# Performance work log

Hardware: AMD Instinct MI355X
Metric: run time of the kernel (lower is better)

## Reference

```python
import jax, jax.numpy as jnp
import numpy as np

J = 24       # num_joints
DIM = 3      # point dim
CD = 128     # c_dim
BN = 4       # bottleneck_size
HPG = 32     # hidden per group (hidden_size=768 / 24)

def setup_inputs() -> dict:
    key = jax.random.key(0)
    ks = jax.random.split(key, 16)
    B, T = 4, 25000
    s = lambda k, shape, fan_in: jax.random.normal(k, shape, jnp.float32) * (1.0 / np.sqrt(fan_in))
    return {
        "p": jax.random.normal(ks[0], (B, J * DIM, T), jnp.float32),
        "z": jax.random.normal(ks[1], (B, 128), jnp.float32),
        "c": jax.random.normal(ks[2], (B, CD), jnp.float32),
        # grouped Conv1d weights stored as (J, out_per_group, in_per_group)
        "W_proj": s(ks[3], (J, BN, CD), CD),          "b_proj": jnp.zeros((J * BN,), jnp.float32),
        "W_p":   s(ks[4], (J, HPG, DIM + BN), DIM+BN), "b_p":   jnp.zeros((J * HPG,), jnp.float32),
        "W0":    s(ks[5], (J, HPG, HPG), HPG),         "b0":    jnp.zeros((J * HPG,), jnp.float32),
        "W1":    s(ks[6], (J, HPG, HPG), HPG),         "b1":    jnp.zeros((J * HPG,), jnp.float32),
        "W2":    s(ks[7], (J, HPG, HPG), HPG),         "b2":    jnp.zeros((J * HPG,), jnp.float32),
        "W_out": s(ks[8], (J, 1, HPG), HPG),           "b_out": jnp.zeros((J,), jnp.float32),
    }

def _gconv(x, W, b):
    # grouped 1x1 conv: x (B,J,Cin,T), W (J,Cout,Cin), b (J*Cout,) -> (B,J,Cout,T)
    y = jnp.einsum('bjit,joi->bjot', x, W)
    return y + b.reshape(1, J, -1, 1)

def reference(p, z, c, W_proj, b_proj, W_p, b_p, W0, b0, W1, b1, W2, b2, W_out, b_out):
    B, _, T = p.shape
    # p.view(B, J, -1, T) then keep last `dim` channels
    p_in = p.reshape(B, J, -1, T)[:, :, -DIM:, :]            # (B,J,3,T)
    # 2D c branch: repeat per joint, grouped proj, broadcast over T
    c_rep = jnp.broadcast_to(c[:, None, :], (B, J, CD))       # (B,J,128)
    c_proj = jnp.einsum('bjc,joc->bjo', c_rep, W_proj) + b_proj.reshape(1, J, BN)
    c_proj = jnp.broadcast_to(c_proj[:, :, :, None], (B, J, BN, T))
    x = jnp.concatenate([p_in, c_proj], axis=2)               # (B,J,3+4,T)
    net = jax.nn.relu(_gconv(x,   W_p, b_p))
    net = jax.nn.relu(_gconv(net, W0,  b0))
    net = jax.nn.relu(_gconv(net, W1,  b1))
    net = jax.nn.relu(_gconv(net, W2,  b2))
    out = _gconv(net, W_out, b_out)                           # (B,J,1,T)
    return out.reshape(B, J, T)                               # logits (B, num_joints, T)
```

## Files before the change

### kernel.cpp

```cpp
#include <hip/hip_runtime.h>
#include <hip/hip_bf16.h>

#define NJ 24
#define TLEN 25000
#define NB 4
#define CHUNKS 20
#define NWPB (CHUNKS*4)
#define NITERS ((TLEN+63)/64)

typedef short short8 __attribute__((ext_vector_type(8)));
typedef short s16x2 __attribute__((ext_vector_type(2)));
typedef float f32x16 __attribute__((ext_vector_type(16)));

union FragU { unsigned u[4]; short8 s; };

__device__ __forceinline__ unsigned pack2(float a, float b){
    unsigned ua = __float_as_uint(a) + 0x8000u;
    unsigned ub = __float_as_uint(b) + 0x8000u;
    return __builtin_amdgcn_perm(ub, ua, 0x07060302u);
}
__device__ __forceinline__ float bflo(unsigned u){
    union { unsigned v; float f; } t; t.v = u << 16; return t.f;
}

__device__ __forceinline__ unsigned pkrelu(unsigned x){
    union { unsigned u; s16x2 v; } a, r;
    a.u = x;
    s16x2 z; z[0] = 0; z[1] = 0;
    r.v = __builtin_elementwise_max(a.v, z);
    return r.u;
}

__device__ __forceinline__ f32x16 mfma(const FragU &a, const FragU &b, f32x16 c){
    return __builtin_amdgcn_mfma_f32_32x32x16_bf16(a.s, b.s, c, 0, 0, 0);
}

__device__ __forceinline__ FragU mk1(unsigned w){
    FragU f; f.u[0] = w; f.u[1] = 0; f.u[2] = 0; f.u[3] = 0; return f;
}

__device__ __forceinline__ void relu_pack(const f32x16 &acc, FragU &k0, FragU &k1){
    unsigned w[8];
    #pragma unroll
    for (int i = 0; i < 8; ++i) w[i] = pkrelu(pack2(acc[2*i], acc[2*i+1]));
    k0.u[0]=w[0]; k0.u[1]=w[1]; k0.u[2]=w[2]; k0.u[3]=w[3];
    k1.u[0]=w[4]; k1.u[1]=w[5]; k1.u[2]=w[6]; k1.u[3]=w[7];
}

__global__ __launch_bounds__(256, 2) void ptf_decoder_kernel(
    const float* __restrict__ p,    const float* __restrict__ c,
    const float* __restrict__ Wproj,const float* __restrict__ bproj,
    const float* __restrict__ Wp,   const float* __restrict__ bp,
    const float* __restrict__ W0,   const float* __restrict__ b0,
    const float* __restrict__ W1,   const float* __restrict__ b1,
    const float* __restrict__ W2,   const float* __restrict__ b2,
    const float* __restrict__ Wout, const float* __restrict__ bout,
    float* __restrict__ out)
{
    __shared__ __align__(16) float ldsW[3][32][36];
    __shared__ __align__(16) float ldsWp[32][8];
    __shared__ __align__(16) float ldsB[3][32];
    __shared__ __align__(16) float ldsWo[32];

    const int tid = threadIdx.x;
    const int bj  = blockIdx.x % (NB*NJ);
    const int sub = blockIdx.x / (NB*NJ);
    const int b   = bj / NJ;
    const int j   = bj % NJ;

    {
        const float* Wl[3] = {W0, W1, W2};
        #pragma unroll
        for (int L = 0; L < 3; ++L) {
            int row = tid >> 3, c4 = tid & 7;
            float4 v = *reinterpret_cast<const float4*>(Wl[L] + ((size_t)(j*32 + row))*32 + c4*4);
            *reinterpret_cast<float4*>(&ldsW[L][row][c4*4]) = v;
        }
        {
            int row = tid >> 3, i8 = tid & 7;
            ldsWp[row][i8] = (i8 < 7) ? Wp[((size_t)(j*32 + row))*7 + i8]
                                      : bp[j*32 + row];
        }
        if      (tid < 32)  ldsB[0][tid]      = b0[j*32 + tid];
        else if (tid < 64)  ldsB[1][tid-32]   = b1[j*32 + tid-32];
        else if (tid < 96)  ldsB[2][tid-64]   = b2[j*32 + tid-64];
        else if (tid < 128) ldsWo[tid-96]     = Wout[j*32 + tid-96];
    }
    __syncthreads();

    const int lane = tid & 63;
    const int row  = lane & 31;
    const int h    = lane >> 5;

    FragU whi[3][2];
    #pragma unroll
    for (int L = 0; L < 3; ++L) {
        #pragma unroll
        for (int kh = 0; kh < 2; ++kh) {
            const int g  = kh*2 + h;
            const int cA = (g >> 1)*4 + (g & 1);
            const float* base = &ldsW[L][row][0];
            float4 x = *reinterpret_cast<const float4*>(base + cA*4);
            float4 y = *reinterpret_cast<const float4*>(base + (cA+2)*4);
            whi[L][kh].u[0] = pack2(x.x, x.y);
            whi[L][kh].u[1] = pack2(x.z, x.w);
            whi[L][kh].u[2] = pack2(y.x, y.y);
            whi[L][kh].u[3] = pack2(y.z, y.w);
        }
    }
    FragU woF[2];
    #pragma unroll
    for (int kh = 0; kh < 2; ++kh) {
        const int g  = kh*2 + h;
        const int cA = (g >> 1)*4 + (g & 1);
        float4 x = *reinterpret_cast<const float4*>(&ldsWo[cA*4]);
        float4 y = *reinterpret_cast<const float4*>(&ldsWo[(cA+2)*4]);
        woF[kh].u[0] = pack2(x.x, x.y);
        woF[kh].u[1] = pack2(x.z, x.w);
        woF[kh].u[2] = pack2(y.x, y.y);
        woF[kh].u[3] = pack2(y.z, y.w);
    }
    FragU wphi;
    {
        float4 x = make_float4(0,0,0,0), y = make_float4(0,0,0,0);
        if (lane < 32) {
            x = *reinterpret_cast<const float4*>(&ldsWp[row][0]);
            y = *reinterpret_cast<const float4*>(&ldsWp[row][4]);
        }
        wphi.u[0] = pack2(x.x, x.y);
        wphi.u[1] = pack2(x.z, x.w);
        wphi.u[2] = pack2(y.x, y.y);
        wphi.u[3] = pack2(y.z, y.w);
    }

    unsigned biasA[3];
    #pragma unroll
    for (int L = 0; L < 3; ++L) {
        float bl = (h == 0) ? ldsB[L][row] : 0.f;
        unsigned t = pack2(bl, 0.f);
        float res = bl - bflo(t);
        biasA[L] = (h == 0) ? pack2(bl, res) : 0u;
    }
    const unsigned ones2 = (h == 0) ? 0x3f803f80u : 0u;

    f32x16 kZero;
    #pragma unroll
    for (int r = 0; r < 16; ++r) kZero[r] = 0.f;

    float cacc0, cacc1, cacc2, cacc3;
    {
        const float* cb  = c + (size_t)b*128;
        const float* wpj = Wproj + (size_t)j*4*128;
        float cl = cb[lane], chv = cb[lane + 64];
        cacc0 = cl*wpj[0*128+lane] + chv*wpj[0*128+lane+64];
        cacc1 = cl*wpj[1*128+lane] + chv*wpj[1*128+lane+64];
        cacc2 = cl*wpj[2*128+lane] + chv*wpj[2*128+lane+64];
        cacc3 = cl*wpj[3*128+lane] + chv*wpj[3*128+lane+64];
        #pragma unroll
        for (int off = 32; off >= 1; off >>= 1) {
            cacc0 += __shfl_xor(cacc0, off, 64);
            cacc1 += __shfl_xor(cacc1, off, 64);
            cacc2 += __shfl_xor(cacc2, off, 64);
            cacc3 += __shfl_xor(cacc3, off, 64);
        }
        cacc0 += bproj[j*4+0]; cacc1 += bproj[j*4+1];
        cacc2 += bproj[j*4+2]; cacc3 += bproj[j*4+3];
    }
    const float c0v = (lane < 32) ? cacc0 : 0.f;
    unsigned wc2h = pack2(cacc1, cacc2);
    unsigned wc3h = pack2(cacc3, 1.0f);
    if (lane >= 32) { wc2h = 0; wc3h = 0; }
    const float bo = bout[j];

    const float* pb0 = p + ((size_t)(b*(NJ*3) + j*3 + 0))*TLEN;
    const float* pb1 = pb0 + TLEN;
    const float* pb2 = pb1 + TLEN;
    float* ob = out + ((size_t)(b*NJ + j))*TLEN;

    const int w0idx = sub*4 + (tid >> 6);

    auto loadP = [&](int itx, float&x0,float&x1,float&x2,float&x3,float&x4,float&x5){
        x0=0.f;x1=0.f;x2=0.f;x3=0.f;x4=0.f;x5=0.f;
        if (itx < NITERS && lane < 32) {
            int tA = itx*64 + lane;
            int tB = tA + 32;
            tA = tA < TLEN ? tA : TLEN-1;
            tB = tB < TLEN ? tB : TLEN-1;
            x0 = pb0[tA]; x1 = pb1[tA]; x2 = pb2[tA];
            x3 = pb0[tB]; x4 = pb1[tB]; x5 = pb2[tB];
        }
    };

    float a0,a1,a2,a3,a4,a5;
    loadP(w0idx, a0,a1,a2,a3,a4,a5);

    for (int it = w0idx; it < NITERS; it += NWPB) {
        float n0,n1,n2,n3,n4,n5;
        loadP(it + NWPB, n0,n1,n2,n3,n4,n5);

        FragU fAh, fBh;
        fAh.u[0] = pack2(a0, a1);  fAh.u[1] = pack2(a2, c0v);
        fBh.u[0] = pack2(a3, a4);  fBh.u[1] = pack2(a5, c0v);
        fAh.u[2]=wc2h; fAh.u[3]=wc3h;
        fBh.u[2]=wc2h; fBh.u[3]=wc3h;

        f32x16 accA, accB;
        accA = mfma(wphi, fAh, kZero);
        accB = mfma(wphi, fBh, kZero);

        #pragma unroll
        for (int L = 0; L < 3; ++L) {
            f32x16 bAcc = mfma(mk1(biasA[L]), mk1(ones2), kZero);
            FragU pA0, pA1, pB0, pB1;
            relu_pack(accA, pA0, pA1);
            relu_pack(accB, pB0, pB1);
            accA = mfma(whi[L][0], pA0, bAcc);
            accB = mfma(whi[L][0], pB0, bAcc);
            accA = mfma(whi[L][1], pA1, accA);
            accB = mfma(whi[L][1], pB1, accB);
        }

        FragU qA0, qA1, qB0, qB1;
        relu_pack(accA, qA0, qA1);
        relu_pack(accB, qB0, qB1);
        f32x16 oA = mfma(woF[0], qA0, kZero);
        f32x16 oB = mfma(woF[0], qB0, kZero);
        oA = mfma(woF[1], qA1, oA);
        oB = mfma(woF[1], qB1, oB);

        int t = it*64 + lane;
        if (t < TLEN) ob[t] = ((lane < 32) ? oA[0] : oB[0]) + bo;

        a0=n0; a1=n1; a2=n2; a3=n3; a4=n4; a5=n5;
    }
}

extern "C" void kernel_launch(void* const* d_in, const int* in_sizes, int n_in,
                              void* d_out, int out_size, void* d_ws, size_t ws_size,
                              hipStream_t stream) {
    const float* p     = (const float*)d_in[0];
    const float* c     = (const float*)d_in[2];
    const float* Wproj = (const float*)d_in[3];
    const float* bproj = (const float*)d_in[4];
    const float* Wp    = (const float*)d_in[5];
    const float* bp    = (const float*)d_in[6];
    const float* W0    = (const float*)d_in[7];
    const float* b0    = (const float*)d_in[8];
    const float* W1    = (const float*)d_in[9];
    const float* b1    = (const float*)d_in[10];
    const float* W2    = (const float*)d_in[11];
    const float* b2    = (const float*)d_in[12];
    const float* Wout  = (const float*)d_in[13];
    const float* bout  = (const float*)d_in[14];
    float* out = (float*)d_out;

    dim3 grid(NB*NJ*CHUNKS), block(256);
    ptf_decoder_kernel<<<grid, block, 0, stream>>>(
        p, c, Wproj, bproj, Wp, bp, W0, b0, W1, b1, W2, b2, Wout, bout, out);
}
```

Baseline: 35.97 us.

## Hoist bias MFMA out of loop and use inline-asm MFMA with manual nops

Computes the per-layer bias accumulator tiles once before the main loop instead of issuing an extra MFMA per layer per iteration. Every MFMA is replaced with an inline-asm version padded with s_nop instructions so that hazards are handled manually. Launch bounds are relaxed to one block per SM-equivalent so the larger register footprint can be held. The fixed nop padding serialises MFMAs and blocks compiler interleaving, and the extra registers may reduce occupancy.

```diff
diff --git a/kernel.cpp b/kernel.cpp
--- a/kernel.cpp
+++ b/kernel.cpp
@@ -31,12 +31,16 @@
     return r.u;
 }
 
-__device__ __forceinline__ f32x16 mfma(const FragU &a, const FragU &b, f32x16 c){
-    return __builtin_amdgcn_mfma_f32_32x32x16_bf16(a.s, b.s, c, 0, 0, 0);
-}
-
-__device__ __forceinline__ FragU mk1(unsigned w){
-    FragU f; f.u[0] = w; f.u[1] = 0; f.u[2] = 0; f.u[3] = 0; return f;
+__device__ __forceinline__ f32x16 mfma_v(const FragU &a, const FragU &b, const f32x16 &c){
+    f32x16 d;
+    asm("s_nop 1\n\t"
+        "v_mfma_f32_32x32x16_bf16 %0, %1, %2, %3\n\t"
+        "s_nop 7\n\t"
+        "s_nop 7\n\t"
+        "s_nop 7"
+        : "=&v"(d)
+        : "v"(a.s), "v"(b.s), "v"(c));
+    return d;
 }
 
 __device__ __forceinline__ void relu_pack(const f32x16 &acc, FragU &k0, FragU &k1){
@@ -47,7 +51,7 @@
     k1.u[0]=w[4]; k1.u[1]=w[5]; k1.u[2]=w[6]; k1.u[3]=w[7];
 }
 
-__global__ __launch_bounds__(256, 2) void ptf_decoder_kernel(
+__global__ __launch_bounds__(256, 1) void ptf_decoder_kernel(
     const float* __restrict__ p,    const float* __restrict__ c,
     const float* __restrict__ Wproj,const float* __restrict__ bproj,
     const float* __restrict__ Wp,   const float* __restrict__ bp,
@@ -133,19 +137,21 @@
         wphi.u[3] = pack2(y.z, y.w);
     }
 
-    unsigned biasA[3];
+    f32x16 kZero;
+    #pragma unroll
+    for (int r = 0; r < 16; ++r) kZero[r] = 0.f;
+
+    f32x16 biasS[3];
     #pragma unroll
     for (int L = 0; L < 3; ++L) {
         float bl = (h == 0) ? ldsB[L][row] : 0.f;
         unsigned t = pack2(bl, 0.f);
         float res = bl - bflo(t);
-        biasA[L] = (h == 0) ? pack2(bl, res) : 0u;
-    }
-    const unsigned ones2 = (h == 0) ? 0x3f803f80u : 0u;
-
-    f32x16 kZero;
-    #pragma unroll
-    for (int r = 0; r < 16; ++r) kZero[r] = 0.f;
+        unsigned biasw = (h == 0) ? pack2(bl, res) : 0u;
+        FragU ba; ba.u[0] = biasw; ba.u[1] = 0; ba.u[2] = 0; ba.u[3] = 0;
+        FragU on; on.u[0] = (h == 0) ? 0x3f803f80u : 0u; on.u[1] = 0; on.u[2] = 0; on.u[3] = 0;
+        biasS[L] = mfma_v(ba, on, kZero);
+    }
 
     float cacc0, cacc1, cacc2, cacc3;
     {
@@ -204,29 +210,27 @@
         fAh.u[2]=wc2h; fAh.u[3]=wc3h;
         fBh.u[2]=wc2h; fBh.u[3]=wc3h;
 
-        f32x16 accA, accB;
-        accA = mfma(wphi, fAh, kZero);
-        accB = mfma(wphi, fBh, kZero);
+        f32x16 accA = mfma_v(wphi, fAh, kZero);
+        f32x16 accB = mfma_v(wphi, fBh, kZero);
 
         #pragma unroll
         for (int L = 0; L < 3; ++L) {
-            f32x16 bAcc = mfma(mk1(biasA[L]), mk1(ones2), kZero);
             FragU pA0, pA1, pB0, pB1;
             relu_pack(accA, pA0, pA1);
             relu_pack(accB, pB0, pB1);
-            accA = mfma(whi[L][0], pA0, bAcc);
-            accB = mfma(whi[L][0], pB0, bAcc);
-            accA = mfma(whi[L][1], pA1, accA);
-            accB = mfma(whi[L][1], pB1, accB);
+            f32x16 tA2 = mfma_v(whi[L][0], pA0, biasS[L]);
+            f32x16 tB2 = mfma_v(whi[L][0], pB0, biasS[L]);
+            accA = mfma_v(whi[L][1], pA1, tA2);
+            accB = mfma_v(whi[L][1], pB1, tB2);
         }
 
         FragU qA0, qA1, qB0, qB1;
         relu_pack(accA, qA0, qA1);
         relu_pack(accB, qB0, qB1);
-        f32x16 oA = mfma(woF[0], qA0, kZero);
-        f32x16 oB = mfma(woF[0], qB0, kZero);
-        oA = mfma(woF[1], qA1, oA);
-        oB = mfma(woF[1], qB1, oB);
+        f32x16 oA = mfma_v(woF[0], qA0, kZero);
+        f32x16 oB = mfma_v(woF[0], qB0, kZero);
+        oA = mfma_v(woF[1], qA1, oA);
+        oB = mfma_v(woF[1], qB1, oB);
 
         int t = it*64 + lane;
         if (t < TLEN) ob[t] = ((lane < 32) ? oA[0] : oB[0]) + bo;
```

Result: slower. 51.51 us (+43.2%).
